# Optimization experiments

Measured on AMD Instinct MI355X. Metric: run time of the kernel, lower is better.

Reference implementation:

```python
import jax, jax.numpy as jnp
import numpy as np
from jax.ops import segment_sum

N_NODES = 50000
N_EDGES = 50000
N_GRAPHS = 1024


def _inv_deg(idx, num_segments):
    deg = segment_sum(jnp.ones(idx.shape[0], jnp.float32), idx, num_segments=num_segments)
    return jnp.where(deg > 0, 1.0 / deg, 0.0)


def hypergraph_conv(x, W, b, node_idx, edge_idx):
    # PyG HypergraphConv (use_attention=False, heads=1, hyperedge_weight=1):
    # out = D^{-1} H B^{-1} H^T (X W) + b
    D = _inv_deg(node_idx, N_NODES)   # inverse node degree [N]
    B = _inv_deg(edge_idx, N_EDGES)   # inverse hyperedge degree [E]
    xl = x @ W                         # [N, out]
    # node -> hyperedge aggregation
    edge_feat = B[:, None] * segment_sum(xl[node_idx], edge_idx, num_segments=N_EDGES)
    # hyperedge -> node aggregation
    out = D[:, None] * segment_sum(edge_feat[edge_idx], node_idx, num_segments=N_NODES)
    return out + b


def global_mean_pool(x, batch):
    s = segment_sum(x, batch, num_segments=N_GRAPHS)
    cnt = segment_sum(jnp.ones(x.shape[0], jnp.float32), batch, num_segments=N_GRAPHS)
    return s / jnp.maximum(cnt, 1.0)[:, None]


def setup_inputs() -> dict:
    key = jax.random.key(0)
    ks = jax.random.split(key, 16)
    F, H = 128, 256
    def lin(k, fi, fo):
        s = 1.0 / np.sqrt(fi)
        k1, k2 = jax.random.split(k)
        return (jax.random.uniform(k1, (fi, fo), jnp.float32, -s, s),
                jax.random.uniform(k2, (fo,), jnp.float32, -s, s))
    W1, b1 = lin(ks[0], F, H)
    W2, b2 = lin(ks[1], H, 2 * H)
    W3, b3 = lin(ks[2], 2 * H, H)
    Wl1, bl1 = lin(ks[3], H, H // 2)
    Wl2, bl2 = lin(ks[4], H // 2, 1)
    x = jax.random.normal(ks[5], (N_NODES, F), jnp.float32)
    hyperedge_index = jax.random.randint(ks[6], (2, 400000), 0, N_EDGES, jnp.int64)
    batch = jnp.sort(jax.random.randint(ks[7], (N_NODES,), 0, N_GRAPHS, jnp.int64))
    return {"x": x, "hyperedge_index": hyperedge_index, "batch": batch,
            "W1": W1, "b1": b1, "W2": W2, "b2": b2, "W3": W3, "b3": b3,
            "Wl1": Wl1, "bl1": bl1, "Wl2": Wl2, "bl2": bl2}


def reference(x, hyperedge_index, batch, W1, b1, W2, b2, W3, b3, Wl1, bl1, Wl2, bl2):
    node_idx, edge_idx = hyperedge_index[0], hyperedge_index[1]
    h = jax.nn.relu(hypergraph_conv(x, W1, b1, node_idx, edge_idx))
    h = jax.nn.relu(hypergraph_conv(h, W2, b2, node_idx, edge_idx))
    h = jax.nn.relu(hypergraph_conv(h, W3, b3, node_idx, edge_idx))
    g = global_mean_pool(h, batch)              # [G, H]
    g = jax.nn.relu(g @ Wl1 + bl1)
    out = g @ Wl2 + bl2                          # [G, 1]
    return out
```

## Files before the change

kernel.cpp:

```cpp
#include <hip/hip_runtime.h>
#include <hip/hip_bf16.h>

#define N_NODES  50000
#define N_EDGES  50000
#define N_INC    400000
#define N_GRAPHS 1024
#define M_PAD    50048
#define SEG_CAP  50176

typedef __bf16 bf16x8 __attribute__((ext_vector_type(8)));
typedef float  f32x4  __attribute__((ext_vector_type(4)));

__device__ __forceinline__ unsigned short f2bf(float f) {
    __hip_bfloat16 h = __float2bfloat16(f);
    return __builtin_bit_cast(unsigned short, h);
}
__device__ __forceinline__ float bflo(unsigned int u) {
    return __builtin_bit_cast(float, u << 16);
}
__device__ __forceinline__ float bfhi(unsigned int u) {
    return __builtin_bit_cast(float, u & 0xffff0000u);
}
__device__ __forceinline__ unsigned int packbf(float a, float b) {
    return (unsigned int)f2bf(a) | ((unsigned int)f2bf(b) << 16);
}
__device__ __forceinline__ void load_lds16(const unsigned short* g, unsigned short* l) {
    __builtin_amdgcn_global_load_lds((const __attribute__((address_space(1))) void*)g,
                                     (__attribute__((address_space(3))) void*)l, 16, 0, 0);
}

#define NB_INC  1563
__global__ __launch_bounds__(256) void normhist_kernel(const int* __restrict__ hei,
                                                       int* __restrict__ nidx, int* __restrict__ eidx,
                                                       unsigned short* __restrict__ rn,
                                                       unsigned short* __restrict__ re,
                                                       int* __restrict__ ndeg_p, int* __restrict__ edeg_p) {
    __shared__ int s32;
    int t = threadIdx.x;
    if (t == 0) s32 = 0;
    __syncthreads();
    int probe = hei[4 * t + 1] | hei[4 * t + 3];
    if (probe) s32 = 1;
    __syncthreads();
    int is32 = s32;
    int i = blockIdx.x * 256 + t;
    if (i < N_INC) {
        int n, e;
        if (is32) { n = hei[i];     e = hei[N_INC + i]; }
        else      { n = hei[2 * i]; e = hei[2 * N_INC + 2 * i]; }
        nidx[i] = n; eidx[i] = e;
        rn[i] = (unsigned short)atomicAdd(&ndeg_p[n << 4], 1);
        re[i] = (unsigned short)atomicAdd(&edeg_p[e << 4], 1);
    }
}

__global__ __launch_bounds__(256) void scan_up_f(const int* __restrict__ edeg_p,
                                                 const int* __restrict__ ndeg_p,
                                                 const int* __restrict__ hei,
                                                 const int* __restrict__ braw,
                                                 int* __restrict__ eoff, int* __restrict__ noff,
                                                 int* __restrict__ goff,
                                                 int* __restrict__ partials) {
    int b = blockIdx.x, t = threadIdx.x;
    if (b >= 98) {
        __shared__ int s32;
        if (t == 0) s32 = 0;
        __syncthreads();
        int probe = hei[4 * t + 1] | hei[4 * t + 3];
        if (probe) s32 = 1;
        __syncthreads();
        int is32 = s32;
        int g = (b - 98) * 256 + t;
        int lo = 0, hi = N_NODES;
        while (lo < hi) {
            int mid = (lo + hi) >> 1;
            int v = is32 ? braw[mid] : braw[2 * mid];
            if (v < g) lo = mid + 1; else hi = mid;
        }
        goff[g] = lo;
        if (g == 1023) goff[1024] = N_NODES;
        return;
    }
    __shared__ int lds[256];
    const int* in; int* outp; int lb;
    if (b < 49) { in = edeg_p; outp = eoff; lb = b; }
    else        { in = ndeg_p; outp = noff; lb = b - 49; }
    int base = lb * 1024 + t * 4;
    int4 v;
    v.x = in[(size_t)(base + 0) << 4];
    v.y = in[(size_t)(base + 1) << 4];
    v.z = in[(size_t)(base + 2) << 4];
    v.w = in[(size_t)(base + 3) << 4];
    int s = v.x + v.y + v.z + v.w;
    lds[t] = s;
    __syncthreads();
    for (int off = 1; off < 256; off <<= 1) {
        int u = (t >= off) ? lds[t - off] : 0;
        __syncthreads();
        lds[t] += u;
        __syncthreads();
    }
    int excl = lds[t] - s;
    if (t == 255) partials[b] = lds[255];
    int4 o;
    o.x = excl;
    o.y = excl + v.x;
    o.z = o.y + v.y;
    o.w = o.z + v.z;
    *(int4*)(outp + base) = o;
}

__global__ __launch_bounds__(256) void scan_down_f(int* __restrict__ eoff,
                                                   int* __restrict__ noff,
                                                   const int* __restrict__ partials) {
    __shared__ int lds[98];
    int b = blockIdx.x, t = threadIdx.x;
    if (t < 98) lds[t] = partials[t];
    __syncthreads();
    if (t < 2) {
        int lo = t * 49, hi = lo + 49;
        int run = 0;
        for (int i = lo; i < hi; ++i) { int x = lds[i]; lds[i] = run; run += x; }
    }
    __syncthreads();
    int* outp; int lb;
    if (b < 49) { outp = eoff; lb = b; }
    else        { outp = noff; lb = b - 49; }
    int base = lb * 1024 + t * 4;
    int p = lds[b];
    int4 v = *(const int4*)(outp + base);
    v.x += p; v.y += p; v.z += p; v.w += p;
    *(int4*)(outp + base) = v;
}

#define NB_CSR  1563
#define NB_CONV 6250
#define NB_W1   128
#define NB_W2   512
#define NB_W3   512
__global__ __launch_bounds__(256) void prep_kernel(const int* __restrict__ nidx,
                                                   const int* __restrict__ eidx,
                                                   const unsigned short* __restrict__ rn,
                                                   const unsigned short* __restrict__ re,
                                                   const int* __restrict__ eoff,
                                                   const int* __restrict__ noff,
                                                   unsigned short* __restrict__ csre,
                                                   unsigned short* __restrict__ csrn,
                                                   const float* __restrict__ x,
                                                   unsigned short* __restrict__ xbf,
                                                   const float* __restrict__ W1, unsigned short* __restrict__ wt1,
                                                   const float* __restrict__ W2, unsigned short* __restrict__ wt2,
                                                   const float* __restrict__ W3, unsigned short* __restrict__ wt3) {
    int b = blockIdx.x, t = threadIdx.x;
    if (b < NB_CSR) {
        int i = b * 256 + t;
        if (i < N_INC) {
            int n = nidx[i], e = eidx[i];
            csre[eoff[e] + re[i]] = (unsigned short)n;
            csrn[noff[n] + rn[i]] = (unsigned short)e;
        }
    } else if (b < NB_CSR + NB_CONV) {
        int i = (b - NB_CSR) * 256 + t;
        float4 v = *(const float4*)(x + 4 * (size_t)i);
        ushort4 o;
        o.x = f2bf(v.x); o.y = f2bf(v.y); o.z = f2bf(v.z); o.w = f2bf(v.w);
        *(ushort4*)(xbf + 4 * (size_t)i) = o;
    } else if (b < NB_CSR + NB_CONV + NB_W1) {
        int i = (b - NB_CSR - NB_CONV) * 256 + t;
        int k = i >> 8, n = i & 255;
        wt1[n * 128 + k] = f2bf(W1[i]);
    } else if (b < NB_CSR + NB_CONV + NB_W1 + NB_W2) {
        int i = (b - NB_CSR - NB_CONV - NB_W1) * 256 + t;
        int k = i >> 9, n = i & 511;
        wt2[n * 256 + k] = f2bf(W2[i]);
    } else {
        int i = (b - NB_CSR - NB_CONV - NB_W1 - NB_W2) * 256 + t;
        int k = i >> 8, n = i & 255;
        wt3[n * 512 + k] = f2bf(W3[i]);
    }
}

template <bool EPI>
__global__ __launch_bounds__(256) void gemm128_kernel(const unsigned short* __restrict__ A,
                                                      const unsigned short* __restrict__ Bt,
                                                      const float* __restrict__ bias,
                                                      unsigned short* __restrict__ C,
                                                      int M, int K, int N) {
    __shared__ unsigned short smem[2 * 128 * 64];
    unsigned short* As = smem;
    unsigned short* Bs = smem + 128 * 64;
    int tid  = threadIdx.x;
    int wave = tid >> 6, lane = tid & 63;

    int nx  = N >> 7;
    int nwg = gridDim.x;
    int bid = blockIdx.x;
    int q = nwg >> 3, r = nwg & 7;
    int xcd = bid & 7, loc = bid >> 3;
    int wg = (xcd < r) ? (xcd * (q + 1) + loc) : (r * (q + 1) + (xcd - r) * q + loc);
    int n0 = (wg % nx) * 128, m0 = (wg / nx) * 128;

    int quad = lane >> 4, fr = lane & 15;
    int wr = wave >> 1, wc = wave & 1;
    int lrow8 = lane >> 3;
    int lcol  = ((lane & 7) ^ lrow8) * 8;

    const unsigned short* gsrc;
    unsigned short* ldst;
    if (wave < 2) { gsrc = A  + (size_t)(m0 + wave * 64) * K;       ldst = As + wave * 64 * 64; }
    else          { gsrc = Bt + (size_t)(n0 + (wave - 2) * 64) * K; ldst = Bs + (wave - 2) * 64 * 64; }

    f32x4 acc[4][4];
#pragma unroll
    for (int s = 0; s < 4; ++s)
#pragma unroll
        for (int c = 0; c < 4; ++c) acc[s][c] = (f32x4){0.f, 0.f, 0.f, 0.f};

    int swz = fr & 7;
    for (int k0 = 0; k0 < K; k0 += 64) {
#pragma unroll
        for (int l = 0; l < 8; ++l) {
            const unsigned short* g = gsrc + (size_t)(l * 8 + lrow8) * K + k0 + lcol;
            load_lds16(g, ldst + l * 8 * 64);
        }
        __syncthreads();
#pragma unroll
        for (int kk = 0; kk < 2; ++kk) {
            int slot = (kk * 4 + quad) ^ swz;
            bf16x8 af[4], bfr[4];
#pragma unroll
            for (int s = 0; s < 4; ++s)
                af[s] = *(const bf16x8*)&As[(wr * 64 + s * 16 + fr) * 64 + slot * 8];
#pragma unroll
            for (int c = 0; c < 4; ++c)
                bfr[c] = *(const bf16x8*)&Bs[(wc * 64 + c * 16 + fr) * 64 + slot * 8];
#pragma unroll
            for (int s = 0; s < 4; ++s)
#pragma unroll
                for (int c = 0; c < 4; ++c)
                    acc[s][c] = __builtin_amdgcn_mfma_f32_16x16x32_bf16(af[s], bfr[c], acc[s][c], 0, 0, 0);
        }
        __syncthreads();
    }

    float bv[4];
#pragma unroll
    for (int c = 0; c < 4; ++c) bv[c] = EPI ? bias[n0 + wc * 64 + c * 16 + fr] : 0.f;
    unsigned short (*Cs)[136] = reinterpret_cast<unsigned short (*)[136]>(smem);
#pragma unroll
    for (int sp = 0; sp < 2; ++sp) {
#pragma unroll
        for (int sl = 0; sl < 2; ++sl) {
#pragma unroll
            for (int c = 0; c < 4; ++c)
#pragma unroll
                for (int r = 0; r < 4; ++r) {
                    float v = acc[sp * 2 + sl][c][r];
                    if (EPI) v = fmaxf(v + bv[c], 0.f);
                    Cs[sl * 32 + wr * 16 + quad * 4 + r][wc * 64 + c * 16 + fr] = f2bf(v);
                }
        }
        __syncthreads();
#pragma unroll
        for (int i = 0; i < 4; ++i) {
            int rl  = i * 16 + (tid >> 4);
            int col = (tid & 15) * 8;
            int gm  = m0 + ((rl & 31) >> 4) * 64 + (sp * 2 + (rl >> 5)) * 16 + (rl & 15);
            if (gm < M) {
                uint4 v = *(const uint4*)&Cs[rl][col];
                *(uint4*)&C[(size_t)gm * N + n0 + col] = v;
            }
        }
        __syncthreads();
    }
}

template <int C, bool BIAS>
__device__ __forceinline__ void seg_bodyN(const unsigned short* __restrict__ in,
                                          const int* __restrict__ offs,
                                          const int* __restrict__ degs_p,
                                          const unsigned short* __restrict__ csr_src,
                                          const float* __restrict__ bias,
                                          unsigned short* __restrict__ outp,
                                          int nseg) {
    constexpr int LPG = C / 8;
    constexpr int SPW = 64 / LPG;
    int wid  = (blockIdx.x * 256 + threadIdx.x) >> 6;
    int lane = threadIdx.x & 63;
    int grp = lane / LPG, lg = lane % LPG;
    int seg = SPW * wid + grp;
    if (SPW * wid >= nseg) return;
    bool segvalid = seg < nseg;
    int deg   = segvalid ? degs_p[(size_t)seg << 4] : 0;
    int start = segvalid ? offs[seg] : 0;
    float dinv = (deg > 0) ? 1.0f / (float)deg : 0.0f;
    int maxdeg = deg;
#pragma unroll
    for (int m = LPG; m < 64; m <<= 1) maxdeg = max(maxdeg, __shfl_xor(maxdeg, m, 64));
    const unsigned short* cs = csr_src + start;
    float acc[8];
#pragma unroll
    for (int q = 0; q < 8; ++q) acc[q] = 0.f;
    size_t lbase = (size_t)lg * 8;

    auto loadrow = [&](int src, unsigned int* v) {
        src = min(src, nseg - 1);
        const unsigned int* p = (const unsigned int*)(in + (size_t)src * C + lbase);
        uint4 t = *(const uint4*)p; v[0] = t.x; v[1] = t.y; v[2] = t.z; v[3] = t.w;
    };
    auto maccum = [&](unsigned int* v, unsigned int msk) {
#pragma unroll
        for (int q = 0; q < 4; ++q) {
            unsigned int x = v[q] & msk;
            acc[2 * q] += bflo(x); acc[2 * q + 1] += bfhi(x);
        }
    };
    auto maccum_full = [&](unsigned int* v) {
#pragma unroll
        for (int q = 0; q < 4; ++q) {
            unsigned int x = v[q];
            acc[2 * q] += bflo(x); acc[2 * q + 1] += bfhi(x);
        }
    };

    int dc = (deg > 0) ? deg - 1 : 0;
    for (int j = 0; j < maxdeg; j += 8) {
        if (j < deg) {
            unsigned int v[8][4];
            int row[8];
#pragma unroll
            for (int u = 0; u < 8; ++u) {
                int jj = min(j + u, dc);
                row[u] = (int)cs[jj];
            }
#pragma unroll
            for (int u = 0; u < 8; ++u) loadrow(row[u], v[u]);
            __asm__ __volatile__("" ::: "memory");
            if (j + 8 <= deg) {
#pragma unroll
                for (int u = 0; u < 8; ++u) maccum_full(v[u]);
            } else {
#pragma unroll
                for (int u = 0; u < 8; ++u) {
                    unsigned int msk = (j + u < deg) ? 0xffffffffu : 0u;
                    maccum(v[u], msk);
                }
            }
        }
    }

    if (!segvalid) return;
    unsigned int o[4];
#pragma unroll
    for (int q = 0; q < 4; ++q) {
        float a = acc[2 * q] * dinv;
        float b = acc[2 * q + 1] * dinv;
        if constexpr (BIAS) {
            a = fmaxf(a + bias[lbase + 2 * q], 0.f);
            b = fmaxf(b + bias[lbase + 2 * q + 1], 0.f);
        }
        o[q] = packbf(a, b);
    }
    *(uint4*)(outp + (size_t)seg * C + lbase) = make_uint4(o[0], o[1], o[2], o[3]);
}

template <int C>
__global__ __launch_bounds__(256) void seg_edge_t(const unsigned short* __restrict__ xl,
                                                  const int* __restrict__ eoff,
                                                  const int* __restrict__ edeg_p,
                                                  const unsigned short* __restrict__ csr_src,
                                                  unsigned short* __restrict__ ef) {
    seg_bodyN<C, false>(xl, eoff, edeg_p, csr_src, nullptr, ef, N_EDGES);
}

template <int C, bool BIAS>
__global__ __launch_bounds__(256) void seg_node_t(const unsigned short* __restrict__ ef,
                                                  const int* __restrict__ noff,
                                                  const int* __restrict__ ndeg_p,
                                                  const unsigned short* __restrict__ csr_src,
                                                  const float* __restrict__ bias,
                                                  unsigned short* __restrict__ hout) {
    seg_bodyN<C, BIAS>(ef, noff, ndeg_p, csr_src, bias, hout, N_NODES);
}

__global__ __launch_bounds__(256) void pool_head_kernel(const unsigned short* __restrict__ h,
                                                        const int* __restrict__ goff,
                                                        const float* __restrict__ Wl1,
                                                        const float* __restrict__ bl1,
                                                        const float* __restrict__ Wl2,
                                                        const float* __restrict__ bl2,
                                                        float* __restrict__ out) {
    __shared__ float xs[256];
    __shared__ float red[128];
    int g = blockIdx.x, t = threadIdx.x;
    int s = goff[g], cnt = goff[g + 1] - s;
    float a0 = 0.f, a1 = 0.f, a2 = 0.f, a3 = 0.f;
    int i = 0;
    for (; i + 4 <= cnt; i += 4) {
        unsigned int u0 = h[(size_t)(s + i + 0) * 256 + t];
        unsigned int u1 = h[(size_t)(s + i + 1) * 256 + t];
        unsigned int u2 = h[(size_t)(s + i + 2) * 256 + t];
        unsigned int u3 = h[(size_t)(s + i + 3) * 256 + t];
        a0 += __builtin_bit_cast(float, u0 << 16);
        a1 += __builtin_bit_cast(float, u1 << 16);
        a2 += __builtin_bit_cast(float, u2 << 16);
        a3 += __builtin_bit_cast(float, u3 << 16);
    }
    for (; i < cnt; ++i) {
        unsigned int u = h[(size_t)(s + i) * 256 + t];
        a0 += __builtin_bit_cast(float, u << 16);
    }
    float acc = (a0 + a1) + (a2 + a3);
    xs[t] = acc / (float)(cnt > 0 ? cnt : 1);
    __syncthreads();
    if (t < 128) {
        float s2 = 0.f;
        for (int f = 0; f < 256; ++f) s2 += xs[f] * Wl1[f * 128 + t];
        s2 = fmaxf(s2 + bl1[t], 0.f);
        red[t] = s2 * Wl2[t];
    }
    __syncthreads();
    for (int off = 64; off > 0; off >>= 1) {
        if (t < off) red[t] += red[t + off];
        __syncthreads();
    }
    if (t == 0) out[g] = red[0] + bl2[0];
}

extern "C" void kernel_launch(void* const* d_in, const int* in_sizes, int n_in,
                              void* d_out, int out_size, void* d_ws, size_t ws_size,
                              hipStream_t stream) {
    const float* x     = (const float*)d_in[0];
    const int* hei     = (const int*)d_in[1];
    const int* braw    = (const int*)d_in[2];
    const float* W1    = (const float*)d_in[3];
    const float* b1    = (const float*)d_in[4];
    const float* W2    = (const float*)d_in[5];
    const float* b2    = (const float*)d_in[6];
    const float* W3    = (const float*)d_in[7];
    const float* b3    = (const float*)d_in[8];
    const float* Wl1   = (const float*)d_in[9];
    const float* bl1   = (const float*)d_in[10];
    const float* Wl2   = (const float*)d_in[11];
    const float* bl2   = (const float*)d_in[12];
    float* out         = (float*)d_out;

    char* w = (char*)d_ws;
    size_t off = 0;
    auto alloc = [&](size_t bytes) { size_t p = off; off += (bytes + 255) & ~(size_t)255; return p; };
    size_t o_edegp = alloc((size_t)SEG_CAP * 16 * 4);
    size_t o_ndegp = alloc((size_t)SEG_CAP * 16 * 4);
    size_t zero_end = off;
    size_t o_eoff = alloc((size_t)SEG_CAP * 4);
    size_t o_noff = alloc((size_t)SEG_CAP * 4);
    size_t o_goff = alloc((size_t)1025 * 4);
    size_t o_part = alloc(128 * 4);
    size_t o_nidx = alloc((size_t)N_INC * 4);
    size_t o_eidx = alloc((size_t)N_INC * 4);
    size_t o_rn   = alloc((size_t)N_INC * 2);
    size_t o_re   = alloc((size_t)N_INC * 2);
    size_t o_csre = alloc((size_t)N_INC * 2 + 64);
    size_t o_csrn = alloc((size_t)N_INC * 2 + 64);
    size_t o_wt1  = alloc((size_t)128 * 256 * 2);
    size_t o_wt2  = alloc((size_t)256 * 512 * 2);
    size_t o_wt3  = alloc((size_t)512 * 256 * 2);
    size_t o_xbf  = alloc((size_t)M_PAD * 128 * 2);
    size_t o_Y    = alloc((size_t)M_PAD * 256 * 2);
    size_t o_H1   = alloc((size_t)M_PAD * 256 * 2);
    size_t o_H2   = alloc((size_t)M_PAD * 512 * 2);
    size_t o_bufE = alloc((size_t)N_EDGES * 256 * 2);

    int* edeg_p = (int*)(w + o_edegp);
    int* ndeg_p = (int*)(w + o_ndegp);
    int* eoff = (int*)(w + o_eoff);
    int* noff = (int*)(w + o_noff);
    int* goff = (int*)(w + o_goff);
    int* part = (int*)(w + o_part);
    int* nidx = (int*)(w + o_nidx);
    int* eidx = (int*)(w + o_eidx);
    unsigned short* rn   = (unsigned short*)(w + o_rn);
    unsigned short* re   = (unsigned short*)(w + o_re);
    unsigned short* csre = (unsigned short*)(w + o_csre);
    unsigned short* csrn = (unsigned short*)(w + o_csrn);
    unsigned short* wt1  = (unsigned short*)(w + o_wt1);
    unsigned short* wt2  = (unsigned short*)(w + o_wt2);
    unsigned short* wt3  = (unsigned short*)(w + o_wt3);
    unsigned short* xbf  = (unsigned short*)(w + o_xbf);
    unsigned short* Y    = (unsigned short*)(w + o_Y);
    unsigned short* H1   = (unsigned short*)(w + o_H1);
    unsigned short* H2   = (unsigned short*)(w + o_H2);
    unsigned short* bufE = (unsigned short*)(w + o_bufE);

    hipMemsetAsync(w, 0, zero_end, stream);
    normhist_kernel<<<NB_INC, 256, 0, stream>>>(hei, nidx, eidx, rn, re, ndeg_p, edeg_p);
    scan_up_f<<<102, 256, 0, stream>>>(edeg_p, ndeg_p, hei, braw, eoff, noff, goff, part);
    scan_down_f<<<98, 256, 0, stream>>>(eoff, noff, part);
    prep_kernel<<<NB_CSR + NB_CONV + NB_W1 + NB_W2 + NB_W3, 256, 0, stream>>>(
        nidx, eidx, rn, re, eoff, noff, csre, csrn, x, xbf, W1, wt1, W2, wt2, W3, wt3);

    int segGrid2 = ((N_NODES + 1) / 2 * 64 + 255) / 256;
    int segGrid4 = ((N_NODES + 3) / 4 * 64 + 255) / 256;

    seg_edge_t<128><<<segGrid4, 256, 0, stream>>>(xbf, eoff, edeg_p, csre, bufE);
    seg_node_t<128, false><<<segGrid4, 256, 0, stream>>>(bufE, noff, ndeg_p, csrn, nullptr, Y);
    {
        dim3 grid((256 / 128) * (M_PAD / 128));
        gemm128_kernel<true><<<grid, 256, 0, stream>>>(Y, wt1, b1, H1, N_NODES, 128, 256);
    }
    seg_edge_t<256><<<segGrid2, 256, 0, stream>>>(H1, eoff, edeg_p, csre, bufE);
    seg_node_t<256, false><<<segGrid2, 256, 0, stream>>>(bufE, noff, ndeg_p, csrn, nullptr, Y);
    {
        dim3 grid((512 / 128) * (M_PAD / 128));
        gemm128_kernel<true><<<grid, 256, 0, stream>>>(Y, wt2, b2, H2, N_NODES, 256, 512);
    }
    {
        dim3 grid((256 / 128) * (M_PAD / 128));
        gemm128_kernel<false><<<grid, 256, 0, stream>>>(H2, wt3, nullptr, Y, N_NODES, 512, 256);
    }
    seg_edge_t<256><<<segGrid2, 256, 0, stream>>>(Y, eoff, edeg_p, csre, bufE);
    seg_node_t<256, true><<<segGrid2, 256, 0, stream>>>(bufE, noff, ndeg_p, csrn, b3, H1);

    pool_head_kernel<<<N_GRAPHS, 256, 0, stream>>>(H1, goff, Wl1, bl1, Wl2, bl2, out);
}
```

Baseline: 393.4 us.

## Slice segment gather across feature chunks so blocks share rows in cache

Replaces the per-segment gather kernel with a feature-sliced version. Each block handles 32 segments over a 32-column slice, and adjacent blocks cover different slices of the same segment block, so gathered rows are meant to be reused through L2. CSR indices are loaded once per lane and broadcast with shuffles, and output goes through nontemporal 8-byte stores. The trade-off is narrower 8-byte loads per row, more blocks, and the index reads being repeated once per slice. The source-row clamp against nseg is also dropped.

```diff
diff --git a/kernel.cpp b/kernel.cpp
--- a/kernel.cpp
+++ b/kernel.cpp
@@ -276,111 +276,78 @@
 }
 
 template <int C, bool BIAS>
-__device__ __forceinline__ void seg_bodyN(const unsigned short* __restrict__ in,
-                                          const int* __restrict__ offs,
-                                          const int* __restrict__ degs_p,
-                                          const unsigned short* __restrict__ csr_src,
-                                          const float* __restrict__ bias,
-                                          unsigned short* __restrict__ outp,
-                                          int nseg) {
-    constexpr int LPG = C / 8;
-    constexpr int SPW = 64 / LPG;
-    int wid  = (blockIdx.x * 256 + threadIdx.x) >> 6;
-    int lane = threadIdx.x & 63;
-    int grp = lane / LPG, lg = lane % LPG;
-    int seg = SPW * wid + grp;
-    if (SPW * wid >= nseg) return;
+__global__ __launch_bounds__(256) void seg_sliced_kernel(const unsigned short* __restrict__ in,
+                                                         const int* __restrict__ offs,
+                                                         const int* __restrict__ degs_p,
+                                                         const unsigned short* __restrict__ csr_src,
+                                                         const float* __restrict__ bias,
+                                                         unsigned short* __restrict__ outp,
+                                                         int nseg) {
+    constexpr int NS = C / 32;
+    int bid = blockIdx.x;
+    int slice, segblock;
+    if (NS == 8) { slice = bid & 7; segblock = bid >> 3; }
+    else         { int x = bid & 7; slice = x & 3; segblock = ((bid >> 3) << 1) | (x >> 2); }
+
+    int wave = threadIdx.x >> 6, lane = threadIdx.x & 63;
+    int grp = lane >> 3, lg = lane & 7;
+    int segbase = (segblock * 4 + wave) * 8;
+    if (segbase >= nseg) return;
+    int seg = segbase + grp;
     bool segvalid = seg < nseg;
     int deg   = segvalid ? degs_p[(size_t)seg << 4] : 0;
     int start = segvalid ? offs[seg] : 0;
     float dinv = (deg > 0) ? 1.0f / (float)deg : 0.0f;
     int maxdeg = deg;
 #pragma unroll
-    for (int m = LPG; m < 64; m <<= 1) maxdeg = max(maxdeg, __shfl_xor(maxdeg, m, 64));
+    for (int m = 8; m < 64; m <<= 1) maxdeg = max(maxdeg, __shfl_xor(maxdeg, m, 64));
     const unsigned short* cs = csr_src + start;
-    float acc[8];
-#pragma unroll
-    for (int q = 0; q < 8; ++q) acc[q] = 0.f;
-    size_t lbase = (size_t)lg * 8;
-
-    auto loadrow = [&](int src, unsigned int* v) {
-        src = min(src, nseg - 1);
-        const unsigned int* p = (const unsigned int*)(in + (size_t)src * C + lbase);
-        uint4 t = *(const uint4*)p; v[0] = t.x; v[1] = t.y; v[2] = t.z; v[3] = t.w;
-    };
-    auto maccum = [&](unsigned int* v, unsigned int msk) {
-#pragma unroll
-        for (int q = 0; q < 4; ++q) {
-            unsigned int x = v[q] & msk;
-            acc[2 * q] += bflo(x); acc[2 * q + 1] += bfhi(x);
-        }
-    };
-    auto maccum_full = [&](unsigned int* v) {
-#pragma unroll
-        for (int q = 0; q < 4; ++q) {
-            unsigned int x = v[q];
-            acc[2 * q] += bflo(x); acc[2 * q + 1] += bfhi(x);
-        }
-    };
+    float acc[4] = {0.f, 0.f, 0.f, 0.f};
+    size_t fbase = (size_t)slice * 32 + lg * 4;
 
     int dc = (deg > 0) ? deg - 1 : 0;
+    int gbase = grp << 3;
     for (int j = 0; j < maxdeg; j += 8) {
         if (j < deg) {
-            unsigned int v[8][4];
+            int my = (int)cs[min(j + lg, dc)];
             int row[8];
 #pragma unroll
-            for (int u = 0; u < 8; ++u) {
-                int jj = min(j + u, dc);
-                row[u] = (int)cs[jj];
-            }
-#pragma unroll
-            for (int u = 0; u < 8; ++u) loadrow(row[u], v[u]);
+            for (int u = 0; u < 8; ++u) row[u] = __shfl(my, gbase + u, 64);
+            uint2 v[8];
+#pragma unroll
+            for (int u = 0; u < 8; ++u)
+                v[u] = *(const uint2*)(in + (size_t)row[u] * C + fbase);
             __asm__ __volatile__("" ::: "memory");
             if (j + 8 <= deg) {
 #pragma unroll
-                for (int u = 0; u < 8; ++u) maccum_full(v[u]);
+                for (int u = 0; u < 8; ++u) {
+                    acc[0] += bflo(v[u].x); acc[1] += bfhi(v[u].x);
+                    acc[2] += bflo(v[u].y); acc[3] += bfhi(v[u].y);
+                }
             } else {
 #pragma unroll
                 for (int u = 0; u < 8; ++u) {
                     unsigned int msk = (j + u < deg) ? 0xffffffffu : 0u;
-                    maccum(v[u], msk);
+                    unsigned int x0 = v[u].x & msk, x1 = v[u].y & msk;
+                    acc[0] += bflo(x0); acc[1] += bfhi(x0);
+                    acc[2] += bflo(x1); acc[3] += bfhi(x1);
                 }
             }
         }
     }
 
     if (!segvalid) return;
-    unsigned int o[4];
-#pragma unroll
-    for (int q = 0; q < 4; ++q) {
-        float a = acc[2 * q] * dinv;
-        float b = acc[2 * q + 1] * dinv;
-        if constexpr (BIAS) {
-            a = fmaxf(a + bias[lbase + 2 * q], 0.f);
-            b = fmaxf(b + bias[lbase + 2 * q + 1], 0.f);
-        }
-        o[q] = packbf(a, b);
-    }
-    *(uint4*)(outp + (size_t)seg * C + lbase) = make_uint4(o[0], o[1], o[2], o[3]);
-}
-
-template <int C>
-__global__ __launch_bounds__(256) void seg_edge_t(const unsigned short* __restrict__ xl,
-                                                  const int* __restrict__ eoff,
-                                                  const int* __restrict__ edeg_p,
-                                                  const unsigned short* __restrict__ csr_src,
-                                                  unsigned short* __restrict__ ef) {
-    seg_bodyN<C, false>(xl, eoff, edeg_p, csr_src, nullptr, ef, N_EDGES);
-}
-
-template <int C, bool BIAS>
-__global__ __launch_bounds__(256) void seg_node_t(const unsigned short* __restrict__ ef,
-                                                  const int* __restrict__ noff,
-                                                  const int* __restrict__ ndeg_p,
-                                                  const unsigned short* __restrict__ csr_src,
-                                                  const float* __restrict__ bias,
-                                                  unsigned short* __restrict__ hout) {
-    seg_bodyN<C, BIAS>(ef, noff, ndeg_p, csr_src, bias, hout, N_NODES);
+    float a0 = acc[0] * dinv, a1 = acc[1] * dinv;
+    float a2 = acc[2] * dinv, a3 = acc[3] * dinv;
+    if constexpr (BIAS) {
+        a0 = fmaxf(a0 + bias[fbase + 0], 0.f);
+        a1 = fmaxf(a1 + bias[fbase + 1], 0.f);
+        a2 = fmaxf(a2 + bias[fbase + 2], 0.f);
+        a3 = fmaxf(a3 + bias[fbase + 3], 0.f);
+    }
+    unsigned long long ov = (unsigned long long)packbf(a0, a1)
+                          | ((unsigned long long)packbf(a2, a3) << 32);
+    __builtin_nontemporal_store(ov, (unsigned long long*)(outp + (size_t)seg * C + fbase));
 }
 
 __global__ __launch_bounds__(256) void pool_head_kernel(const unsigned short* __restrict__ h,
@@ -498,17 +465,18 @@
     prep_kernel<<<NB_CSR + NB_CONV + NB_W1 + NB_W2 + NB_W3, 256, 0, stream>>>(
         nidx, eidx, rn, re, eoff, noff, csre, csrn, x, xbf, W1, wt1, W2, wt2, W3, wt3);
 
-    int segGrid2 = ((N_NODES + 1) / 2 * 64 + 255) / 256;
-    int segGrid4 = ((N_NODES + 3) / 4 * 64 + 255) / 256;
-
-    seg_edge_t<128><<<segGrid4, 256, 0, stream>>>(xbf, eoff, edeg_p, csre, bufE);
-    seg_node_t<128, false><<<segGrid4, 256, 0, stream>>>(bufE, noff, ndeg_p, csrn, nullptr, Y);
+    int sb = (N_NODES + 31) / 32;
+    int grid256 = sb * 8;
+    int grid128 = sb * 4;
+
+    seg_sliced_kernel<128, false><<<grid128, 256, 0, stream>>>(xbf, eoff, edeg_p, csre, nullptr, bufE, N_EDGES);
+    seg_sliced_kernel<128, false><<<grid128, 256, 0, stream>>>(bufE, noff, ndeg_p, csrn, nullptr, Y, N_NODES);
     {
         dim3 grid((256 / 128) * (M_PAD / 128));
         gemm128_kernel<true><<<grid, 256, 0, stream>>>(Y, wt1, b1, H1, N_NODES, 128, 256);
     }
-    seg_edge_t<256><<<segGrid2, 256, 0, stream>>>(H1, eoff, edeg_p, csre, bufE);
-    seg_node_t<256, false><<<segGrid2, 256, 0, stream>>>(bufE, noff, ndeg_p, csrn, nullptr, Y);
+    seg_sliced_kernel<256, false><<<grid256, 256, 0, stream>>>(H1, eoff, edeg_p, csre, nullptr, bufE, N_EDGES);
+    seg_sliced_kernel<256, false><<<grid256, 256, 0, stream>>>(bufE, noff, ndeg_p, csrn, nullptr, Y, N_NODES);
     {
         dim3 grid((512 / 128) * (M_PAD / 128));
         gemm128_kernel<true><<<grid, 256, 0, stream>>>(Y, wt2, b2, H2, N_NODES, 256, 512);
@@ -517,8 +485,8 @@
         dim3 grid((256 / 128) * (M_PAD / 128));
         gemm128_kernel<false><<<grid, 256, 0, stream>>>(H2, wt3, nullptr, Y, N_NODES, 512, 256);
     }
-    seg_edge_t<256><<<segGrid2, 256, 0, stream>>>(Y, eoff, edeg_p, csre, bufE);
-    seg_node_t<256, true><<<segGrid2, 256, 0, stream>>>(bufE, noff, ndeg_p, csrn, b3, H1);
+    seg_sliced_kernel<256, false><<<grid256, 256, 0, stream>>>(Y, eoff, edeg_p, csre, nullptr, bufE, N_EDGES);
+    seg_sliced_kernel<256, true><<<grid256, 256, 0, stream>>>(bufE, noff, ndeg_p, csrn, b3, H1, N_NODES);
 
     pool_head_kernel<<<N_GRAPHS, 256, 0, stream>>>(H1, goff, Wl1, bl1, Wl2, bl2, out);
 }
```

After: 465.0 us. +18.2%, slower.
